# Optimization experiments

Hardware: AMD Instinct MI355X
Metric: run time of the kernel (lower is better)

The kernel has to match this reference:

```python
import jax, jax.numpy as jnp
import numpy as np

IN_FEATURES = 512
OUT_FEATURES = 512
GRID_SIZE = 8
BATCH = 4096


def setup_inputs() -> dict:
    key = jax.random.key(0)
    k_x, k_sw, k_ba = jax.random.split(key, 3)
    x = jax.random.normal(k_x, (BATCH, IN_FEATURES), dtype=jnp.float32)
    spline_weight = jax.random.normal(k_sw, (OUT_FEATURES, IN_FEATURES, GRID_SIZE), dtype=jnp.float32)
    base_activation = jax.random.normal(k_ba, (OUT_FEATURES, IN_FEATURES), dtype=jnp.float32)
    grid_points = jnp.linspace(-1.0, 1.0, GRID_SIZE, dtype=jnp.float32)
    return {"x": x, "spline_weight": spline_weight, "base_activation": base_activation, "grid_points": grid_points}


def _bspline_basis(d):
    # piecewise cubic: d = |x - grid|
    inner = 1.0 - 6.0 * d * d + 6.0 * d * d * d
    outer = 2.0 * (1.0 - d) ** 3
    return jnp.where(d < 0.5, inner, jnp.where(d < 1.0, outer, jnp.zeros_like(d)))


def reference(x, spline_weight, base_activation, grid_points):
    x_norm = jnp.tanh(x)                                  # (B, in)
    d = jnp.abs(x_norm[:, :, None] - grid_points)          # (B, in, grid)
    basis = _bspline_basis(d)                              # (B, in, grid)
    # sum over grid then in_features, weighted by spline_weight (out, in, grid)
    spline_out = jnp.einsum('big,oig->bo', basis, spline_weight)
    base_out = x_norm @ base_activation.T                  # (B, out)
    return spline_out + 0.1 * base_out
```

## Files before the change

kernel.cpp:

```cpp
#include <hip/hip_runtime.h>

#define IN_F   512
#define OUT_F  512
#define GRID_N 8
#define BATCH  4096
#define KDIM   (IN_F * 9)
#define SPLITK 4
#define KCHUNK (KDIM / SPLITK)
#define BKSTEPS (KCHUNK / 32)

typedef __fp16 half8 __attribute__((ext_vector_type(8)));
typedef float  f32x4 __attribute__((ext_vector_type(4)));

__device__ __forceinline__ void gload16(const void* gsrc, void* ldst) {
  __builtin_amdgcn_global_load_lds(
      (__attribute__((address_space(1))) void*)(void*)gsrc,
      (__attribute__((address_space(3))) void*)ldst, 16, 0, 0);
}

__global__ void feat_kernel(const float* __restrict__ x, const float* __restrict__ grid,
                            __fp16* __restrict__ A) {
  const int idx = blockIdx.x * 256 + threadIdx.x;
  const float xn = tanhf(x[idx]);
  const int b = idx >> 9;
  const int i = idx & (IN_F - 1);
  __fp16* arow = A + (size_t)b * KDIM + i;
#pragma unroll
  for (int g = 0; g < GRID_N; ++g) {
    const float d  = fabsf(xn - grid[g]);
    const float dd = d * d;
    const float inner = 1.0f - 6.0f * dd + 6.0f * dd * d;
    const float om = 1.0f - d;
    const float outer = 2.0f * om * om * om;
    const float bas = (d < 0.5f) ? inner : ((d < 1.0f) ? outer : 0.0f);
    arow[g * IN_F] = (__fp16)bas;
  }
  arow[8 * IN_F] = (__fp16)xn;
}

__global__ void wt_kernel(const float* __restrict__ sw, const float* __restrict__ ba,
                          __fp16* __restrict__ W) {
  const int idx = blockIdx.x * 256 + threadIdx.x;
  const int o = idx >> 9;
  const int i = idx & (IN_F - 1);
  const float* swp = sw + (size_t)idx * GRID_N;
  __fp16* wrow = W + (size_t)o * KDIM + i;
#pragma unroll
  for (int g = 0; g < GRID_N; ++g) wrow[g * IN_F] = (__fp16)swp[g];
  wrow[8 * IN_F] = (__fp16)(0.1f * ba[idx]);
}

__global__ __launch_bounds__(256) void gemm_kernel(const __fp16* __restrict__ A,
                                                   const __fp16* __restrict__ W,
                                                   float* __restrict__ P) {
  __shared__ __align__(16) __fp16 As[128 * 32];
  __shared__ __align__(16) __fp16 Bs[128 * 32];
  const int tid  = threadIdx.x;
  const int lane = tid & 63;
  const int wv   = tid >> 6;
  const int wm   = wv >> 1;
  const int wn   = wv & 1;
  const int m0 = blockIdx.x * 128;
  const int n0 = blockIdx.y * 128;
  const int kbase = blockIdx.z * KCHUNK;

  const int e0 = wv * 512 + lane * 8;
  const int r0 = e0 >> 5, c0 = e0 & 31;
  const int r1 = (e0 + 2048) >> 5, c1 = (e0 + 2048) & 31;
  const __fp16* Ag0 = A + (size_t)(m0 + r0) * KDIM + kbase + c0;
  const __fp16* Ag1 = A + (size_t)(m0 + r1) * KDIM + kbase + c1;
  const __fp16* Wg0 = W + (size_t)(n0 + r0) * KDIM + kbase + c0;
  const __fp16* Wg1 = W + (size_t)(n0 + r1) * KDIM + kbase + c1;
  __fp16* lA0 = &As[wv * 512];
  __fp16* lA1 = &As[wv * 512 + 2048];
  __fp16* lB0 = &Bs[wv * 512];
  __fp16* lB1 = &Bs[wv * 512 + 2048];

  const int fr = lane & 15;
  const int g4 = lane >> 4;

  f32x4 acc[4][4] = {};

  for (int kt = 0; kt < BKSTEPS; ++kt) {
    gload16(Ag0, lA0);
    gload16(Ag1, lA1);
    gload16(Wg0, lB0);
    gload16(Wg1, lB1);
    Ag0 += 32; Ag1 += 32; Wg0 += 32; Wg1 += 32;
    __syncthreads();
    half8 a[4], b[4];
#pragma unroll
    for (int mi = 0; mi < 4; ++mi)
      a[mi] = *(const half8*)&As[(wm * 64 + mi * 16 + fr) * 32 + g4 * 8];
#pragma unroll
    for (int ni = 0; ni < 4; ++ni)
      b[ni] = *(const half8*)&Bs[(wn * 64 + ni * 16 + fr) * 32 + g4 * 8];
#pragma unroll
    for (int mi = 0; mi < 4; ++mi)
#pragma unroll
      for (int ni = 0; ni < 4; ++ni)
        acc[mi][ni] = __builtin_amdgcn_mfma_f32_16x16x32_f16(a[mi], b[ni], acc[mi][ni], 0, 0, 0);
    __syncthreads();
  }

  float* Pp = P + (size_t)blockIdx.z * (BATCH * OUT_F);
#pragma unroll
  for (int mi = 0; mi < 4; ++mi) {
#pragma unroll
    for (int ni = 0; ni < 4; ++ni) {
      const int row = m0 + wm * 64 + mi * 16 + g4 * 4;
      const int col = n0 + wn * 64 + ni * 16 + fr;
#pragma unroll
      for (int rg = 0; rg < 4; ++rg)
        Pp[(size_t)(row + rg) * OUT_F + col] = acc[mi][ni][rg];
    }
  }
}

__global__ void reduce_kernel(const float* __restrict__ P, float* __restrict__ out) {
  const int idx = blockIdx.x * 256 + threadIdx.x;
  const f32x4* P4 = (const f32x4*)P;
  const int stride = (BATCH * OUT_F) / 4;
  f32x4 s = P4[idx] + P4[idx + stride] + P4[idx + 2 * stride] + P4[idx + 3 * stride];
  ((f32x4*)out)[idx] = s;
}

extern "C" void kernel_launch(void* const* d_in, const int* in_sizes, int n_in,
                              void* d_out, int out_size, void* d_ws, size_t ws_size,
                              hipStream_t stream) {
  const float* x  = (const float*)d_in[0];
  const float* sw = (const float*)d_in[1];
  const float* ba = (const float*)d_in[2];
  const float* gp = (const float*)d_in[3];
  float* out = (float*)d_out;

  char* ws = (char*)d_ws;
  const size_t A_BYTES = (size_t)BATCH * KDIM * 2;
  const size_t W_BYTES = (size_t)OUT_F * KDIM * 2;
  __fp16* A = (__fp16*)ws;
  __fp16* W = (__fp16*)(ws + A_BYTES);
  float*  P = (float*)(ws + A_BYTES + W_BYTES);

  feat_kernel<<<(BATCH * IN_F) / 256, 256, 0, stream>>>(x, gp, A);
  wt_kernel<<<(OUT_F * IN_F) / 256, 256, 0, stream>>>(sw, ba, W);
  gemm_kernel<<<dim3(BATCH / 128, OUT_F / 128, SPLITK), 256, 0, stream>>>(A, W, P);
  reduce_kernel<<<(BATCH * OUT_F) / 4 / 256, 256, 0, stream>>>(P, out);
}
```

Baseline: 117.6 us.

## Double GEMM K-tile with XOR-swizzled LDS and merge prep kernels

Raises the GEMM K-tile from 32 to 64, halving the number of barrier-separated iterations. LDS is laid out with an XOR swizzle on 16-byte chunks to avoid bank conflicts on the fragment reads. The feature and weight-conversion kernels are merged into one launch to save launch overhead. LDS use per block doubles and more fragments are held in registers, which may lower occupancy.

```diff
diff --git a/kernel.cpp b/kernel.cpp
--- a/kernel.cpp
+++ b/kernel.cpp
@@ -7,7 +7,8 @@
 #define KDIM   (IN_F * 9)
 #define SPLITK 4
 #define KCHUNK (KDIM / SPLITK)
-#define BKSTEPS (KCHUNK / 32)
+#define BK     64
+#define BKSTEPS (KCHUNK / BK)
 
 typedef __fp16 half8 __attribute__((ext_vector_type(8)));
 typedef float  f32x4 __attribute__((ext_vector_type(4)));
@@ -18,43 +19,42 @@
       (__attribute__((address_space(3))) void*)ldst, 16, 0, 0);
 }
 
-__global__ void feat_kernel(const float* __restrict__ x, const float* __restrict__ grid,
-                            __fp16* __restrict__ A) {
-  const int idx = blockIdx.x * 256 + threadIdx.x;
-  const float xn = tanhf(x[idx]);
-  const int b = idx >> 9;
-  const int i = idx & (IN_F - 1);
-  __fp16* arow = A + (size_t)b * KDIM + i;
+__global__ void prep_kernel(const float* __restrict__ x, const float* __restrict__ grid,
+                            const float* __restrict__ sw, const float* __restrict__ ba,
+                            __fp16* __restrict__ A, __fp16* __restrict__ W) {
+  const int bid = blockIdx.x;
+  if (bid < (BATCH * IN_F) / 256) {
+    const int idx = bid * 256 + threadIdx.x;
+    const float xn = tanhf(x[idx]);
+    const int b = idx >> 9;
+    const int i = idx & (IN_F - 1);
+    __fp16* arow = A + (size_t)b * KDIM + i;
 #pragma unroll
-  for (int g = 0; g < GRID_N; ++g) {
-    const float d  = fabsf(xn - grid[g]);
-    const float dd = d * d;
-    const float inner = 1.0f - 6.0f * dd + 6.0f * dd * d;
-    const float om = 1.0f - d;
-    const float outer = 2.0f * om * om * om;
-    const float bas = (d < 0.5f) ? inner : ((d < 1.0f) ? outer : 0.0f);
-    arow[g * IN_F] = (__fp16)bas;
+    for (int g = 0; g < GRID_N; ++g) {
+      const float d  = fabsf(xn - grid[g]);
+      const float dd = d * d;
+      const float inner = 1.0f - 6.0f * dd + 6.0f * dd * d;
+      const float om = 1.0f - d;
+      const float outer = 2.0f * om * om * om;
+      const float bas = (d < 0.5f) ? inner : ((d < 1.0f) ? outer : 0.0f);
+      arow[g * IN_F] = (__fp16)bas;
+    }
+    arow[8 * IN_F] = (__fp16)xn;
+  } else {
+    const int idx = (bid - (BATCH * IN_F) / 256) * 256 + threadIdx.x;
+    const float* swp = sw + (size_t)idx * GRID_N;
+    __fp16* wrow = W + (size_t)(idx >> 9) * KDIM + (idx & (IN_F - 1));
+#pragma unroll
+    for (int g = 0; g < GRID_N; ++g) wrow[g * IN_F] = (__fp16)swp[g];
+    wrow[8 * IN_F] = (__fp16)(0.1f * ba[idx]);
   }
-  arow[8 * IN_F] = (__fp16)xn;
-}
-
-__global__ void wt_kernel(const float* __restrict__ sw, const float* __restrict__ ba,
-                          __fp16* __restrict__ W) {
-  const int idx = blockIdx.x * 256 + threadIdx.x;
-  const int o = idx >> 9;
-  const int i = idx & (IN_F - 1);
-  const float* swp = sw + (size_t)idx * GRID_N;
-  __fp16* wrow = W + (size_t)o * KDIM + i;
-#pragma unroll
-  for (int g = 0; g < GRID_N; ++g) wrow[g * IN_F] = (__fp16)swp[g];
-  wrow[8 * IN_F] = (__fp16)(0.1f * ba[idx]);
 }
 
 __global__ __launch_bounds__(256) void gemm_kernel(const __fp16* __restrict__ A,
                                                    const __fp16* __restrict__ W,
                                                    float* __restrict__ P) {
-  __shared__ __align__(16) __fp16 As[128 * 32];
-  __shared__ __align__(16) __fp16 Bs[128 * 32];
+  __shared__ __align__(16) __fp16 As[128 * BK];
+  __shared__ __align__(16) __fp16 Bs[128 * BK];
   const int tid  = threadIdx.x;
   const int lane = tid & 63;
   const int wv   = tid >> 6;
@@ -64,42 +64,59 @@
   const int n0 = blockIdx.y * 128;
   const int kbase = blockIdx.z * KCHUNK;
 
-  const int e0 = wv * 512 + lane * 8;
-  const int r0 = e0 >> 5, c0 = e0 & 31;
-  const int r1 = (e0 + 2048) >> 5, c1 = (e0 + 2048) & 31;
-  const __fp16* Ag0 = A + (size_t)(m0 + r0) * KDIM + kbase + c0;
-  const __fp16* Ag1 = A + (size_t)(m0 + r1) * KDIM + kbase + c1;
-  const __fp16* Wg0 = W + (size_t)(n0 + r0) * KDIM + kbase + c0;
-  const __fp16* Wg1 = W + (size_t)(n0 + r1) * KDIM + kbase + c1;
-  __fp16* lA0 = &As[wv * 512];
-  __fp16* lA1 = &As[wv * 512 + 2048];
-  __fp16* lB0 = &Bs[wv * 512];
-  __fp16* lB1 = &Bs[wv * 512 + 2048];
+  const __fp16* Ag[4];
+  const __fp16* Wg[4];
+  __fp16* lA[4];
+  __fp16* lB[4];
+#pragma unroll
+  for (int j = 0; j < 4; ++j) {
+    const int t = wv * 4 + j;
+    const int r = t * 8 + (lane >> 3);
+    const int cs = (((lane & 7) ^ (r & 7))) * 8;
+    Ag[j] = A + (size_t)(m0 + r) * KDIM + kbase + cs;
+    Wg[j] = W + (size_t)(n0 + r) * KDIM + kbase + cs;
+    lA[j] = &As[t * 512];
+    lB[j] = &Bs[t * 512];
+  }
 
   const int fr = lane & 15;
   const int g4 = lane >> 4;
+  const int xr = fr & 7;
 
   f32x4 acc[4][4] = {};
 
   for (int kt = 0; kt < BKSTEPS; ++kt) {
-    gload16(Ag0, lA0);
-    gload16(Ag1, lA1);
-    gload16(Wg0, lB0);
-    gload16(Wg1, lB1);
-    Ag0 += 32; Ag1 += 32; Wg0 += 32; Wg1 += 32;
+#pragma unroll
+    for (int j = 0; j < 4; ++j) {
+      gload16(Ag[j], lA[j]);
+      gload16(Wg[j], lB[j]);
+      Ag[j] += BK; Wg[j] += BK;
+    }
     __syncthreads();
-    half8 a[4], b[4];
+
+    half8 a[2][4], b[2][4];
 #pragma unroll
-    for (int mi = 0; mi < 4; ++mi)
-      a[mi] = *(const half8*)&As[(wm * 64 + mi * 16 + fr) * 32 + g4 * 8];
+    for (int ks = 0; ks < 2; ++ks) {
 #pragma unroll
-    for (int ni = 0; ni < 4; ++ni)
-      b[ni] = *(const half8*)&Bs[(wn * 64 + ni * 16 + fr) * 32 + g4 * 8];
+      for (int mi = 0; mi < 4; ++mi) {
+        const int row = wm * 64 + mi * 16 + fr;
+        const int ch = (ks * 4 + g4) ^ xr;
+        a[ks][mi] = *(const half8*)&As[row * BK + ch * 8];
+      }
 #pragma unroll
-    for (int mi = 0; mi < 4; ++mi)
+      for (int ni = 0; ni < 4; ++ni) {
+        const int row = wn * 64 + ni * 16 + fr;
+        const int ch = (ks * 4 + g4) ^ xr;
+        b[ks][ni] = *(const half8*)&Bs[row * BK + ch * 8];
+      }
+    }
 #pragma unroll
-      for (int ni = 0; ni < 4; ++ni)
-        acc[mi][ni] = __builtin_amdgcn_mfma_f32_16x16x32_f16(a[mi], b[ni], acc[mi][ni], 0, 0, 0);
+    for (int ks = 0; ks < 2; ++ks)
+#pragma unroll
+      for (int mi = 0; mi < 4; ++mi)
+#pragma unroll
+        for (int ni = 0; ni < 4; ++ni)
+          acc[mi][ni] = __builtin_amdgcn_mfma_f32_16x16x32_f16(a[ks][mi], b[ks][ni], acc[mi][ni], 0, 0, 0);
     __syncthreads();
   }
 
@@ -141,8 +158,9 @@
   __fp16* W = (__fp16*)(ws + A_BYTES);
   float*  P = (float*)(ws + A_BYTES + W_BYTES);
 
-  feat_kernel<<<(BATCH * IN_F) / 256, 256, 0, stream>>>(x, gp, A);
-  wt_kernel<<<(OUT_F * IN_F) / 256, 256, 0, stream>>>(sw, ba, W);
+  const int FEAT_BLKS = (BATCH * IN_F) / 256;
+  const int WT_BLKS   = (OUT_F * IN_F) / 256;
+  prep_kernel<<<FEAT_BLKS + WT_BLKS, 256, 0, stream>>>(x, gp, sw, ba, A, W);
   gemm_kernel<<<dim3(BATCH / 128, OUT_F / 128, SPLITK), 256, 0, stream>>>(A, W, P);
   reduce_kernel<<<(BATCH * OUT_F) / 4 / 256, 256, 0, stream>>>(P, out);
 }
```

After: 109.4 us. 7.0% less time.
